# Performance work log

Hardware: AMD Instinct MI355X
Metric: run time of the kernel (lower is better)

Reference implementation:

```python
import jax, jax.numpy as jnp
import numpy as np

T, N, L = 512, 128, 256           # encoder steps, batch, decode steps
KV, VS = 128, 128                 # key_size, value_size
EMB, HID, VOC = 256, 512, 34


def _lstm_cell(x, h, c, W_ih, W_hh, b_ih, b_hh):
    # PyTorch LSTMCell gate order: i, f, g, o
    g = x @ W_ih.T + b_ih + h @ W_hh.T + b_hh
    i, f, gg, o = jnp.split(g, 4, axis=-1)
    c2 = jax.nn.sigmoid(f) * c + jax.nn.sigmoid(i) * jnp.tanh(gg)
    h2 = jax.nn.sigmoid(o) * jnp.tanh(c2)
    return h2, c2


def setup_inputs() -> dict:
    k = jax.random.key(0)
    ks = jax.random.split(k, 16)
    s = 0.05
    return {
        "key": jax.random.normal(ks[0], (T, N, KV), jnp.float32),
        "values": jax.random.normal(ks[1], (T, N, VS), jnp.float32),
        "lens": jax.random.randint(ks[2], (N,), 1, T + 1),
        "text": jax.random.randint(ks[3], (N, L), 0, VOC),
        "emb": jax.random.normal(ks[4], (VOC, EMB), jnp.float32) * s,
        "W_ih1": jax.random.normal(ks[5], (4 * HID, EMB + VS), jnp.float32) * s,
        "W_hh1": jax.random.normal(ks[6], (4 * HID, HID), jnp.float32) * s,
        "b_ih1": jnp.zeros((4 * HID,), jnp.float32),
        "b_hh1": jnp.zeros((4 * HID,), jnp.float32),
        "W_ih2": jax.random.normal(ks[7], (4 * KV, HID), jnp.float32) * s,
        "W_hh2": jax.random.normal(ks[8], (4 * KV, KV), jnp.float32) * s,
        "b_ih2": jnp.zeros((4 * KV,), jnp.float32),
        "b_hh2": jnp.zeros((4 * KV,), jnp.float32),
        "W_out": jax.random.normal(ks[9], (VOC, KV + VS), jnp.float32) * s,
        "b_out": jnp.zeros((VOC,), jnp.float32),
    }


def reference(key, values, lens, text, emb, W_ih1, W_hh1, b_ih1, b_hh1,
              W_ih2, W_hh2, b_ih2, b_hh2, W_out, b_out):
    # key/values: (T, N, 128); teacher-forced decode over L steps.
    pad_mask = jnp.arange(T)[None, :] >= lens[:, None]        # (N, T)
    embs = emb[text]                                          # (N, L, EMB)
    embs = jnp.transpose(embs, (1, 0, 2))                     # (L, N, EMB)

    def step(carry, e_t):
        h1, c1, h2, c2, ctx = carry
        x = jnp.concatenate([e_t, ctx], axis=-1)
        h1, c1 = _lstm_cell(x, h1, c1, W_ih1, W_hh1, b_ih1, b_hh1)
        h2, c2 = _lstm_cell(h1, h2, c2, W_ih2, W_hh2, b_ih2, b_hh2)
        # masked bmm attention: energy (N, T)
        energy = jnp.einsum('tnk,nk->nt', key, h2)
        energy = jnp.where(pad_mask, -1e9, energy)
        attn = jax.nn.softmax(energy, axis=1)
        ctx = jnp.einsum('nt,tnv->nv', attn, values)
        pred = jnp.concatenate([h2, ctx], axis=-1) @ W_out.T + b_out
        return (h1, c1, h2, c2, ctx), pred

    init = (jnp.zeros((N, HID)), jnp.zeros((N, HID)),
            jnp.zeros((N, KV)), jnp.zeros((N, KV)),
            jnp.zeros((N, VS)))
    _, preds = jax.lax.scan(step, init, embs)                 # (L, N, VOC)
    return jnp.transpose(preds, (1, 0, 2))                    # (N, L, VOC)
```

## Files before the change

kernel.cpp:

```cpp
#include <hip/hip_runtime.h>
#include <hip/hip_cooperative_groups.h>
#include <math.h>

#define LDEC 256
#define VOCD 34
#define SPIN_MAX 2000000u

typedef __attribute__((ext_vector_type(8))) short bf16x8;
typedef __attribute__((ext_vector_type(4))) float f32x4;

#define OFF_W1H  0u
#define OFF_W1L  2621440u
#define OFF_W2H  5242880u
#define OFF_W2L  5898240u
#define OFF_EG   6553600u
#define OFF_B2   6832128u
#define OFF_WOT  6834176u
#define OFF_H1P  6868992u
#define OFF_H2P  7393280u
#define OFF_CTXP 7524352u
#define OFF_C1   7589888u
#define OFF_C2   7852032u
#define OFF_FLG  7917568u

__device__ __forceinline__ float sigf(float x) { return 1.0f / (1.0f + expf(-x)); }
__device__ __forceinline__ unsigned short f2b(float x) {
  unsigned int u = __float_as_uint(x);
  unsigned int r = (u + 0x7FFFu + ((u >> 16) & 1u)) >> 16;
  return (unsigned short)r;
}
__device__ __forceinline__ float b2f(unsigned short h) {
  return __uint_as_float(((unsigned int)h) << 16);
}
__device__ __forceinline__ unsigned packf(float x) {
  unsigned short hi = f2b(x);
  unsigned short lo = f2b(x - b2f(hi));
  return ((unsigned)hi << 16) | (unsigned)lo;
}
__device__ __forceinline__ float unpackf(unsigned p) {
  return b2f((unsigned short)(p >> 16)) + b2f((unsigned short)(p & 0xffffu));
}
__device__ __forceinline__ unsigned aload(const unsigned* p) {
  return __hip_atomic_load((unsigned*)p, __ATOMIC_RELAXED, __HIP_MEMORY_SCOPE_SYSTEM);
}
__device__ __forceinline__ void astore(unsigned* p, unsigned v) {
  __hip_atomic_store(p, v, __ATOMIC_RELAXED, __HIP_MEMORY_SCOPE_SYSTEM);
}
__device__ __forceinline__ void unpack8(const unsigned* p, bf16x8& xh, bf16x8& xl) {
#pragma unroll
  for (int j = 0; j < 8; j++) {
    unsigned v = p[j];
    xh[j] = (short)(v >> 16);
    xl[j] = (short)(v & 0xffffu);
  }
}

__device__ __forceinline__ void flag_arrive(unsigned* f) {
  __builtin_amdgcn_s_waitcnt(0);
  __hip_atomic_fetch_add(f, 1u, __ATOMIC_RELAXED, __HIP_MEMORY_SCOPE_SYSTEM);
}
__device__ __forceinline__ void flag_wait(unsigned* f, unsigned target, unsigned* budget) {
  if (*budget == 0) return;
  while (aload(f) < target) {
    __builtin_amdgcn_s_sleep(2);
    if (--(*budget) == 0) break;
  }
  asm volatile("" ::: "memory");
}

__global__ __launch_bounds__(256) void pack_w1(const float* __restrict__ Wih1,
                                               const float* __restrict__ Whh1,
                                               unsigned short* __restrict__ W1H,
                                               unsigned short* __restrict__ W1L) {
  int idx = blockIdx.x * 256 + threadIdx.x;
  int m = idx / 640, k = idx % 640;
  int u = m >> 2, q = m & 3;
  int g = q * 512 + u;
  float v = (k < 128) ? Wih1[g * 384 + 256 + k] : Whh1[g * 512 + (k - 128)];
  unsigned short hi = f2b(v);
  W1H[idx] = hi;
  W1L[idx] = f2b(v - b2f(hi));
}

__global__ __launch_bounds__(256) void pack_w2(const float* __restrict__ Wih2,
                                               const float* __restrict__ Whh2,
                                               unsigned short* __restrict__ W2H,
                                               unsigned short* __restrict__ W2L) {
  int idx = blockIdx.x * 256 + threadIdx.x;
  int m = idx / 640, k = idx % 640;
  int u = m >> 2, q = m & 3;
  int g = q * 128 + u;
  float v = (k < 512) ? Wih2[g * 512 + k] : Whh2[g * 128 + (k - 512)];
  unsigned short hi = f2b(v);
  W2H[idx] = hi;
  W2L[idx] = f2b(v - b2f(hi));
}

__global__ __launch_bounds__(256) void pack_eg(const float* __restrict__ emb,
                                               const float* __restrict__ Wih1,
                                               const float* __restrict__ bih1,
                                               const float* __restrict__ bhh1,
                                               float* __restrict__ EG) {
  int idx = blockIdx.x * 256 + threadIdx.x;
  int v = idx >> 11, m = idx & 2047;
  int u = m >> 2, q = m & 3;
  int g = q * 512 + u;
  float acc = bih1[g] + bhh1[g];
  const float* e = emb + v * 256;
  const float* w = Wih1 + g * 384;
  for (int k = 0; k < 256; k++) acc += e[k] * w[k];
  EG[idx] = acc;
}

__global__ __launch_bounds__(256) void pack_misc(const float* __restrict__ Wout,
                                                 const float* __restrict__ bih2,
                                                 const float* __restrict__ bhh2,
                                                 float* __restrict__ WoT,
                                                 float* __restrict__ B2) {
  int idx = blockIdx.x * 256 + threadIdx.x;
  if (idx < 8704) {
    int k = idx / 34, v = idx % 34;
    WoT[idx] = Wout[v * 256 + k];
  } else if (idx < 9216) {
    int m = idx - 8704;
    int u = m >> 2, q = m & 3;
    int g = q * 128 + u;
    B2[m] = bih2[g] + bhh2[g];
  }
}

__device__ __forceinline__ void dev_phaseA(
    int gang, int gidx, int tid, int t, int rp, int wp,
    const unsigned short* __restrict__ W1H, const unsigned short* __restrict__ W1L,
    const float* __restrict__ EG, const int* __restrict__ text,
    const unsigned* __restrict__ CTXP, unsigned* __restrict__ H1P,
    float* __restrict__ C1)
{
  __shared__ unsigned xsh[16 * 644];
  __shared__ float bredA[4096];

  const int wid = tid >> 6, lane = tid & 63;
  const int l15 = lane & 15, lg = lane >> 4;
  const int gr = wid >> 2, gwid = wid & 3;
  const int kb0 = gwid * 160;

  {
    int kcol = tid & 15, nl = (tid >> 4) & 15, rep = tid >> 8;
    int n = gang * 16 + nl;
    const unsigned* ctxp = CTXP + n * 128;
    const unsigned* h1p  = H1P + rp * 65536 + n * 512;
#pragma unroll
    for (int j = 0; j < 10; j++) {
      int k = rep * 160 + j * 16 + kcol;
      unsigned v = (k < 128) ? aload(ctxp + k) : aload(h1p + (k - 128));
      xsh[nl * 644 + k] = v;
    }
  }
  __syncthreads();

  const int mt = gidx * 4 + gr;
  {
    const unsigned short* whp = W1H + (size_t)(mt * 16 + l15) * 640 + kb0 + lg * 8;
    const unsigned short* wlp = W1L + (size_t)(mt * 16 + l15) * 640 + kb0 + lg * 8;
    const unsigned* xrow = xsh + l15 * 644 + kb0 + lg * 8;
    f32x4 a0 = {0.0f, 0.0f, 0.0f, 0.0f};
    f32x4 a1 = {0.0f, 0.0f, 0.0f, 0.0f};
    f32x4 a2 = {0.0f, 0.0f, 0.0f, 0.0f};
#pragma unroll
    for (int ks = 0; ks < 5; ks++) {
      unsigned parr[8];
      *(uint4*)parr       = *(const uint4*)(xrow + ks * 32);
      *(uint4*)(parr + 4) = *(const uint4*)(xrow + ks * 32 + 4);
      bf16x8 xh_, xl_;
      unpack8(parr, xh_, xl_);
      bf16x8 wh_ = *(const bf16x8*)(whp + ks * 32);
      bf16x8 wl_ = *(const bf16x8*)(wlp + ks * 32);
      a0 = __builtin_amdgcn_mfma_f32_16x16x32_bf16(wh_, xh_, a0, 0, 0, 0);
      a1 = __builtin_amdgcn_mfma_f32_16x16x32_bf16(wl_, xh_, a1, 0, 0, 0);
      a2 = __builtin_amdgcn_mfma_f32_16x16x32_bf16(wh_, xl_, a2, 0, 0, 0);
    }
    f32x4 acc = a0 + a1;
    acc = acc + a2;
#pragma unroll
    for (int q = 0; q < 4; q++) bredA[gr * 1024 + q * 256 + gwid * 64 + lane] = acc[q];
  }
  __syncthreads();

  if (gwid == 0) {
    const float* br = bredA + gr * 1024;
    int n = gang * 16 + l15;
    int tok = text[n * LDEC + t];
    f32x4 egv = *(const f32x4*)(EG + (size_t)tok * 2048 + mt * 16 + lg * 4);
    float g0 = br[lane]       + br[64 + lane]  + br[128 + lane] + br[192 + lane] + egv[0];
    float g1 = br[256 + lane] + br[320 + lane] + br[384 + lane] + br[448 + lane] + egv[1];
    float g2 = br[512 + lane] + br[576 + lane] + br[640 + lane] + br[704 + lane] + egv[2];
    float g3 = br[768 + lane] + br[832 + lane] + br[896 + lane] + br[960 + lane] + egv[3];
    float ig = sigf(g0), fg = sigf(g1), gg = tanhf(g2), og = sigf(g3);
    int u = mt * 4 + lg;
    float c = fg * C1[u * 128 + n] + ig * gg;
    float h = og * tanhf(c);
    C1[u * 128 + n] = c;
    astore(H1P + wp * 65536 + n * 512 + u, packf(h));
  }
  __syncthreads();
}

__device__ __forceinline__ void dev_phaseB(
    int gang, int gidx, int tid, int rp, int wp,
    const unsigned short* __restrict__ W2H, const unsigned short* __restrict__ W2L,
    const float* __restrict__ B2,
    const unsigned* __restrict__ H1P, unsigned* __restrict__ H2P,
    float* __restrict__ C2)
{
  __shared__ float bredB[1024];
  const int wid = tid >> 6, lane = tid & 63;
  const int l15 = lane & 15, lg = lane >> 4;
  const int mtB = gidx;
  if (tid < 256) {
    const int kb0 = wid * 160;
    int n = gang * 16 + l15;
    const unsigned* x1 = H1P + wp * 65536 + n * 512;
    const unsigned* x2 = H2P + rp * 16384 + n * 128;
    const unsigned short* whp = W2H + (size_t)(mtB * 16 + l15) * 640 + kb0 + lg * 8;
    const unsigned short* wlp = W2L + (size_t)(mtB * 16 + l15) * 640 + kb0 + lg * 8;
    f32x4 a0 = {0.0f, 0.0f, 0.0f, 0.0f};
    f32x4 a1 = {0.0f, 0.0f, 0.0f, 0.0f};
    f32x4 a2 = {0.0f, 0.0f, 0.0f, 0.0f};
#pragma unroll
    for (int ks = 0; ks < 5; ks++) {
      int kb = kb0 + ks * 32;
      unsigned parr[8];
      const unsigned* src = (kb < 512) ? (x1 + kb + lg * 8) : (x2 + (kb - 512) + lg * 8);
#pragma unroll
      for (int j = 0; j < 8; j++) parr[j] = aload(src + j);
      bf16x8 xh_, xl_;
      unpack8(parr, xh_, xl_);
      bf16x8 wh_ = *(const bf16x8*)(whp + ks * 32);
      bf16x8 wl_ = *(const bf16x8*)(wlp + ks * 32);
      a0 = __builtin_amdgcn_mfma_f32_16x16x32_bf16(wh_, xh_, a0, 0, 0, 0);
      a1 = __builtin_amdgcn_mfma_f32_16x16x32_bf16(wl_, xh_, a1, 0, 0, 0);
      a2 = __builtin_amdgcn_mfma_f32_16x16x32_bf16(wh_, xl_, a2, 0, 0, 0);
    }
    f32x4 acc = a0 + a1;
    acc = acc + a2;
#pragma unroll
    for (int q = 0; q < 4; q++) bredB[q * 256 + wid * 64 + lane] = acc[q];
  }
  __syncthreads();
  if (tid < 64) {
    f32x4 b2v = *(const f32x4*)(B2 + mtB * 16 + lg * 4);
    float g0 = bredB[lane]       + bredB[64 + lane]  + bredB[128 + lane] + bredB[192 + lane] + b2v[0];
    float g1 = bredB[256 + lane] + bredB[320 + lane] + bredB[384 + lane] + bredB[448 + lane] + b2v[1];
    float g2 = bredB[512 + lane] + bredB[576 + lane] + bredB[640 + lane] + bredB[704 + lane] + b2v[2];
    float g3 = bredB[768 + lane] + bredB[832 + lane] + bredB[896 + lane] + bredB[960 + lane] + b2v[3];
    int n = gang * 16 + l15;
    int u = mtB * 4 + lg;
    float c = sigf(g1) * C2[u * 128 + n] + sigf(g0) * tanhf(g2);
    float h = sigf(g3) * tanhf(c);
    C2[u * 128 + n] = c;
    astore(H2P + wp * 16384 + n * 128 + u, packf(h));
  }
  __syncthreads();
}

__device__ __forceinline__ void dev_phaseC(
    int n, int tid, int len, int t, int wp,
    const float* __restrict__ key, const float* __restrict__ values,
    const unsigned* __restrict__ H2P, const float* __restrict__ WoT,
    const float* __restrict__ bout, unsigned* __restrict__ CTXP,
    float* __restrict__ out)
{
  __shared__ float cred[4224];
  __shared__ float red[1024];
  __shared__ float es[512];
  __shared__ float h2s[128];
  __shared__ float ctxs[128];
  __shared__ float pr[68];

  if (tid < 128) h2s[tid] = unpackf(aload(H2P + wp * 16384 + n * 128 + tid));
  __syncthreads();
  float lmax = -1e30f;
  if (tid < len) {
    const float4* kr = (const float4*)(key + ((size_t)tid * 128 + n) * 128);
    float acc = 0.0f;
#pragma unroll 8
    for (int k = 0; k < 32; k++) {
      float4 kv = kr[k];
      acc += kv.x * h2s[4 * k] + kv.y * h2s[4 * k + 1] + kv.z * h2s[4 * k + 2] + kv.w * h2s[4 * k + 3];
    }
    es[tid] = acc;
    lmax = acc;
  }
  red[tid] = lmax; __syncthreads();
  for (int s = 512; s > 0; s >>= 1) { if (tid < s) red[tid] = fmaxf(red[tid], red[tid + s]); __syncthreads(); }
  float m = red[0];
  __syncthreads();
  float ls = 0.0f;
  if (tid < len) {
    float p = expf(es[tid] - m);
    es[tid] = p;
    ls = p;
  }
  red[tid] = ls; __syncthreads();
  for (int s = 512; s > 0; s >>= 1) { if (tid < s) red[tid] += red[tid + s]; __syncthreads(); }
  float S = red[0];
  __syncthreads();
  {
    int v4 = (tid & 31) * 4, tp = tid >> 5;
    float ax = 0.0f, ay = 0.0f, az = 0.0f, aw = 0.0f;
#pragma unroll 2
    for (int tt = tp; tt < len; tt += 32) {
      float p = es[tt];
      const float4 vv = *(const float4*)(values + ((size_t)tt * 128 + n) * 128 + v4);
      ax += p * vv.x; ay += p * vv.y; az += p * vv.z; aw += p * vv.w;
    }
    float4 a4 = {ax, ay, az, aw};
    *(float4*)&cred[tp * 132 + v4] = a4;
  }
  __syncthreads();
  if (tid < 128) {
    float s4 = 0.0f;
#pragma unroll 8
    for (int tp2 = 0; tp2 < 32; tp2++) s4 += cred[tp2 * 132 + tid];
    float cv = s4 / S;
    ctxs[tid] = cv;
    astore(CTXP + n * 128 + tid, packf(cv));
  }
  __syncthreads();
  if (tid < 68) {
    int vv = tid % 34, part = tid / 34;
    const float* src = part ? ctxs : h2s;
    const float* wcol = WoT + (part ? 128 * 34 : 0);
    float a = 0.0f;
#pragma unroll 8
    for (int k2 = 0; k2 < 128; k2++) a += src[k2] * wcol[k2 * 34 + vv];
    pr[tid] = a;
  }
  __syncthreads();
  if (tid < 34) {
    out[(size_t)n * (LDEC * VOCD) + t * VOCD + tid] = bout[tid] + pr[tid] + pr[34 + tid];
  }
  __syncthreads();
}

__global__ void __launch_bounds__(1024, 4) kA(
    const unsigned short* __restrict__ W1H, const unsigned short* __restrict__ W1L,
    const float* __restrict__ EG, const int* __restrict__ text,
    const unsigned* __restrict__ CTXP, unsigned* __restrict__ H1P,
    float* __restrict__ C1, int t, int rp, int wp)
{
  dev_phaseA(blockIdx.x >> 5, blockIdx.x & 31, threadIdx.x, t, rp, wp,
             W1H, W1L, EG, text, CTXP, H1P, C1);
}
__global__ void __launch_bounds__(256) kB(
    const unsigned short* __restrict__ W2H, const unsigned short* __restrict__ W2L,
    const float* __restrict__ B2, const unsigned* __restrict__ H1P,
    unsigned* __restrict__ H2P, float* __restrict__ C2, int rp, int wp)
{
  dev_phaseB(blockIdx.x >> 5, blockIdx.x & 31, threadIdx.x, rp, wp,
             W2H, W2L, B2, H1P, H2P, C2);
}
__global__ void __launch_bounds__(1024, 4) kC(
    const float* __restrict__ key, const float* __restrict__ values,
    const int* __restrict__ lens, const unsigned* __restrict__ H2P,
    const float* __restrict__ WoT, const float* __restrict__ bout,
    unsigned* __restrict__ CTXP, float* __restrict__ out, int t, int wp)
{
  int n = blockIdx.x;
  dev_phaseC(n, threadIdx.x, lens[n], t, wp, key, values, H2P, WoT, bout, CTXP, out);
}

__global__ void __launch_bounds__(1024, 4) decoder_coop(
    const float* __restrict__ key, const float* __restrict__ values,
    const int* __restrict__ lens, const int* __restrict__ text,
    const float* __restrict__ EG, const float* __restrict__ B2,
    const float* __restrict__ WoT, const float* __restrict__ bout,
    const unsigned short* __restrict__ W1H, const unsigned short* __restrict__ W1L,
    const unsigned short* __restrict__ W2H, const unsigned short* __restrict__ W2L,
    unsigned* __restrict__ CTXP, unsigned* __restrict__ H1P,
    unsigned* __restrict__ H2P, float* __restrict__ C1, float* __restrict__ C2,
    unsigned* __restrict__ FLG, float* __restrict__ out)
{
  const int bid = blockIdx.x, tid = threadIdx.x;
  const int gang = bid >> 5, gidx = bid & 31;
  unsigned* fA = FLG + gang * 16;
  unsigned* fB = FLG + 128 + gang * 16;
  unsigned* fC = FLG + 256 + gang * 16;
  const int cn = gang * 16 + gidx;
  const int clen = (gidx < 16) ? lens[cn] : 0;

  unsigned budget = SPIN_MAX;

  for (int t = 0; t < LDEC; t++) {
    const int wp = t & 1, rp = (t + 1) & 1;

    dev_phaseA(gang, gidx, tid, t, rp, wp, W1H, W1L, EG, text, CTXP, H1P, C1);
    if (tid == 0) { flag_arrive(fA); flag_wait(fA, 32u * (t + 1), &budget); }
    __syncthreads();

    dev_phaseB(gang, gidx, tid, rp, wp, W2H, W2L, B2, H1P, H2P, C2);
    if (tid == 0) flag_arrive(fB);
    if (gidx < 16) {
      if (tid == 0) flag_wait(fB, 32u * (t + 1), &budget);
      __syncthreads();
      dev_phaseC(cn, tid, clen, t, wp, key, values, H2P, WoT, bout, CTXP, out);
      if (tid == 0) flag_arrive(fC);
    }
    if (tid == 0) flag_wait(fC, 16u * (t + 1), &budget);
    __syncthreads();
  }

  if (tid == 0 && budget == 0) out[0] = 7.0e6f;
}

extern "C" void kernel_launch(void* const* d_in, const int* in_sizes, int n_in,
                              void* d_out, int out_size, void* d_ws, size_t ws_size,
                              hipStream_t stream) {
  const float* key    = (const float*)d_in[0];
  const float* values = (const float*)d_in[1];
  const int*   lens   = (const int*)d_in[2];
  const int*   text   = (const int*)d_in[3];
  const float* emb    = (const float*)d_in[4];
  const float* Wih1   = (const float*)d_in[5];
  const float* Whh1   = (const float*)d_in[6];
  const float* bih1   = (const float*)d_in[7];
  const float* bhh1   = (const float*)d_in[8];
  const float* Wih2   = (const float*)d_in[9];
  const float* Whh2   = (const float*)d_in[10];
  const float* bih2   = (const float*)d_in[11];
  const float* bhh2   = (const float*)d_in[12];
  const float* Wout   = (const float*)d_in[13];
  const float* bout   = (const float*)d_in[14];

  char* ws = (char*)d_ws;
  unsigned short* W1H = (unsigned short*)(ws + OFF_W1H);
  unsigned short* W1L = (unsigned short*)(ws + OFF_W1L);
  unsigned short* W2H = (unsigned short*)(ws + OFF_W2H);
  unsigned short* W2L = (unsigned short*)(ws + OFF_W2L);
  float* EG   = (float*)(ws + OFF_EG);
  float* B2   = (float*)(ws + OFF_B2);
  float* WoT  = (float*)(ws + OFF_WOT);
  unsigned* H1P  = (unsigned*)(ws + OFF_H1P);
  unsigned* H2P  = (unsigned*)(ws + OFF_H2P);
  unsigned* CTXP = (unsigned*)(ws + OFF_CTXP);
  float* C1   = (float*)(ws + OFF_C1);
  float* C2   = (float*)(ws + OFF_C2);
  unsigned* FLG = (unsigned*)(ws + OFF_FLG);
  float* out  = (float*)d_out;

  hipMemsetAsync(CTXP, 0, 65536, stream);
  hipMemsetAsync((char*)H1P + 262144, 0, 262144, stream);
  hipMemsetAsync((char*)H2P + 65536, 0, 65536, stream);
  hipMemsetAsync(C1,  0, 262144, stream);
  hipMemsetAsync(C2,  0, 65536, stream);
  hipMemsetAsync(FLG, 0, 2048, stream);

  pack_w1  <<<5120, 256, 0, stream>>>(Wih1, Whh1, W1H, W1L);
  pack_w2  <<<1280, 256, 0, stream>>>(Wih2, Whh2, W2H, W2L);
  pack_eg  <<<272,  256, 0, stream>>>(emb, Wih1, bih1, bhh1, EG);
  pack_misc<<<36,   256, 0, stream>>>(Wout, bih2, bhh2, WoT, B2);

  int maxBlk = 0;
  hipError_t qerr = hipOccupancyMaxActiveBlocksPerMultiprocessor(
      &maxBlk, (const void*)decoder_coop, 1024, 0);
  bool coop_ok = (qerr == hipSuccess && maxBlk >= 1);

  if (coop_ok) {
    void* args[] = {
      (void*)&key, (void*)&values, (void*)&lens, (void*)&text,
      (void*)&EG, (void*)&B2, (void*)&WoT, (void*)&bout,
      (void*)&W1H, (void*)&W1L, (void*)&W2H, (void*)&W2L,
      (void*)&CTXP, (void*)&H1P, (void*)&H2P, (void*)&C1, (void*)&C2,
      (void*)&FLG, (void*)&out
    };
    hipError_t err = hipLaunchCooperativeKernel((const void*)decoder_coop,
                                                dim3(256), dim3(1024), args, 0, stream);
    if (err == hipSuccess) return;
  }

  for (int t = 0; t < LDEC; t++) {
    const int wp = t & 1, rp = (t + 1) & 1;
    kA<<<256, 1024, 0, stream>>>(W1H, W1L, EG, text, CTXP, H1P, C1, t, rp, wp);
    kB<<<256, 256,  0, stream>>>(W2H, W2L, B2, H1P, H2P, C2, rp, wp);
    kC<<<128, 1024, 0, stream>>>(key, values, lens, H2P, WoT, bout, CTXP, out, t, wp);
  }
}
```

Before: 9.203 ms.

## Redistribute LSTM phase work across fewer blocks and prestage h1 into shared memory

Phase A now runs on 16 blocks per gang, each handling two m-tiles, and phase B on 8 blocks per gang using all 16 waves with an LDS-staged input. The next step's h1 is staged into shared memory right after phase A, so it overlaps with the phase-B and phase-C waits, and only the ctx part is reloaded at the start of each step. Phase-C shared buffers are unioned with the phase-B staging buffer to keep LDS within budget. The cost is fewer active blocks per phase, so each participating block does more serial work.

```diff
diff --git a/kernel.cpp b/kernel.cpp
--- a/kernel.cpp
+++ b/kernel.cpp
@@ -129,40 +129,42 @@
   }
 }
 
-__device__ __forceinline__ void dev_phaseA(
-    int gang, int gidx, int tid, int t, int rp, int wp,
+__device__ __forceinline__ void stage_h1(int gang, int tid, int rbuf,
+                                         unsigned* xshA, const unsigned* __restrict__ H1P) {
+  int kcol = tid & 15, nl = (tid >> 4) & 15, rep = tid >> 8;
+  int n = gang * 16 + nl;
+  const unsigned* h1p = H1P + rbuf * 65536 + n * 512;
+#pragma unroll
+  for (int j = 0; j < 10; j++) {
+    int k = rep * 160 + j * 16 + kcol;
+    if (k >= 128) xshA[nl * 644 + k] = aload(h1p + (k - 128));
+  }
+}
+__device__ __forceinline__ void stage_ctx(int gang, int tid,
+                                          unsigned* xshA, const unsigned* __restrict__ CTXP) {
+  int kcol = tid & 15, nl = (tid >> 4) & 15, rep = tid >> 8;
+  int n = gang * 16 + nl;
+  if (rep == 0) {
+#pragma unroll
+    for (int j = 0; j < 8; j++) {
+      int k = j * 16 + kcol;
+      xshA[nl * 644 + k] = aload(CTXP + n * 128 + k);
+    }
+  }
+}
+
+__device__ __forceinline__ void A_tile(
+    int gang, int mt, int gr, int gwid, int lane, int l15, int lg, int tid, int t,
+    const unsigned* __restrict__ xshA, float* bred,
     const unsigned short* __restrict__ W1H, const unsigned short* __restrict__ W1L,
     const float* __restrict__ EG, const int* __restrict__ text,
-    const unsigned* __restrict__ CTXP, unsigned* __restrict__ H1P,
-    float* __restrict__ C1)
-{
-  __shared__ unsigned xsh[16 * 644];
-  __shared__ float bredA[4096];
-
-  const int wid = tid >> 6, lane = tid & 63;
-  const int l15 = lane & 15, lg = lane >> 4;
-  const int gr = wid >> 2, gwid = wid & 3;
+    unsigned* __restrict__ H1P, float* __restrict__ C1, int wp)
+{
   const int kb0 = gwid * 160;
-
-  {
-    int kcol = tid & 15, nl = (tid >> 4) & 15, rep = tid >> 8;
-    int n = gang * 16 + nl;
-    const unsigned* ctxp = CTXP + n * 128;
-    const unsigned* h1p  = H1P + rp * 65536 + n * 512;
-#pragma unroll
-    for (int j = 0; j < 10; j++) {
-      int k = rep * 160 + j * 16 + kcol;
-      unsigned v = (k < 128) ? aload(ctxp + k) : aload(h1p + (k - 128));
-      xsh[nl * 644 + k] = v;
-    }
-  }
-  __syncthreads();
-
-  const int mt = gidx * 4 + gr;
   {
     const unsigned short* whp = W1H + (size_t)(mt * 16 + l15) * 640 + kb0 + lg * 8;
     const unsigned short* wlp = W1L + (size_t)(mt * 16 + l15) * 640 + kb0 + lg * 8;
-    const unsigned* xrow = xsh + l15 * 644 + kb0 + lg * 8;
+    const unsigned* xrow = xshA + l15 * 644 + kb0 + lg * 8;
     f32x4 a0 = {0.0f, 0.0f, 0.0f, 0.0f};
     f32x4 a1 = {0.0f, 0.0f, 0.0f, 0.0f};
     f32x4 a2 = {0.0f, 0.0f, 0.0f, 0.0f};
@@ -182,12 +184,11 @@
     f32x4 acc = a0 + a1;
     acc = acc + a2;
 #pragma unroll
-    for (int q = 0; q < 4; q++) bredA[gr * 1024 + q * 256 + gwid * 64 + lane] = acc[q];
-  }
-  __syncthreads();
-
+    for (int q = 0; q < 4; q++) bred[gr * 1024 + q * 256 + gwid * 64 + lane] = acc[q];
+  }
+  __syncthreads();
   if (gwid == 0) {
-    const float* br = bredA + gr * 1024;
+    const float* br = bred + gr * 1024;
     int n = gang * 16 + l15;
     int tok = text[n * LDEC + t];
     f32x4 egv = *(const f32x4*)(EG + (size_t)tok * 2048 + mt * 16 + lg * 4);
@@ -205,34 +206,26 @@
   __syncthreads();
 }
 
-__device__ __forceinline__ void dev_phaseB(
-    int gang, int gidx, int tid, int rp, int wp,
+__device__ __forceinline__ void B_tile(
+    int gang, int mtB, int gr, int gwid, int lane, int l15, int lg,
+    const unsigned* __restrict__ xshB, float* bred,
     const unsigned short* __restrict__ W2H, const unsigned short* __restrict__ W2L,
-    const float* __restrict__ B2,
-    const unsigned* __restrict__ H1P, unsigned* __restrict__ H2P,
-    float* __restrict__ C2)
-{
-  __shared__ float bredB[1024];
-  const int wid = tid >> 6, lane = tid & 63;
-  const int l15 = lane & 15, lg = lane >> 4;
-  const int mtB = gidx;
-  if (tid < 256) {
-    const int kb0 = wid * 160;
-    int n = gang * 16 + l15;
-    const unsigned* x1 = H1P + wp * 65536 + n * 512;
-    const unsigned* x2 = H2P + rp * 16384 + n * 128;
+    const float* __restrict__ B2, unsigned* __restrict__ H2P,
+    float* __restrict__ C2, int wp)
+{
+  const int kb0 = gwid * 160;
+  {
     const unsigned short* whp = W2H + (size_t)(mtB * 16 + l15) * 640 + kb0 + lg * 8;
     const unsigned short* wlp = W2L + (size_t)(mtB * 16 + l15) * 640 + kb0 + lg * 8;
+    const unsigned* xrow = xshB + l15 * 644 + kb0 + lg * 8;
     f32x4 a0 = {0.0f, 0.0f, 0.0f, 0.0f};
     f32x4 a1 = {0.0f, 0.0f, 0.0f, 0.0f};
     f32x4 a2 = {0.0f, 0.0f, 0.0f, 0.0f};
 #pragma unroll
     for (int ks = 0; ks < 5; ks++) {
-      int kb = kb0 + ks * 32;
       unsigned parr[8];
-      const unsigned* src = (kb < 512) ? (x1 + kb + lg * 8) : (x2 + (kb - 512) + lg * 8);
-#pragma unroll
-      for (int j = 0; j < 8; j++) parr[j] = aload(src + j);
+      *(uint4*)parr       = *(const uint4*)(xrow + ks * 32);
+      *(uint4*)(parr + 4) = *(const uint4*)(xrow + ks * 32 + 4);
       bf16x8 xh_, xl_;
       unpack8(parr, xh_, xl_);
       bf16x8 wh_ = *(const bf16x8*)(whp + ks * 32);
@@ -244,16 +237,17 @@
     f32x4 acc = a0 + a1;
     acc = acc + a2;
 #pragma unroll
-    for (int q = 0; q < 4; q++) bredB[q * 256 + wid * 64 + lane] = acc[q];
-  }
-  __syncthreads();
-  if (tid < 64) {
+    for (int q = 0; q < 4; q++) bred[gr * 1024 + q * 256 + gwid * 64 + lane] = acc[q];
+  }
+  __syncthreads();
+  if (gwid == 0) {
+    const float* br = bred + gr * 1024;
+    int n = gang * 16 + l15;
     f32x4 b2v = *(const f32x4*)(B2 + mtB * 16 + lg * 4);
-    float g0 = bredB[lane]       + bredB[64 + lane]  + bredB[128 + lane] + bredB[192 + lane] + b2v[0];
-    float g1 = bredB[256 + lane] + bredB[320 + lane] + bredB[384 + lane] + bredB[448 + lane] + b2v[1];
-    float g2 = bredB[512 + lane] + bredB[576 + lane] + bredB[640 + lane] + bredB[704 + lane] + b2v[2];
-    float g3 = bredB[768 + lane] + bredB[832 + lane] + bredB[896 + lane] + bredB[960 + lane] + b2v[3];
-    int n = gang * 16 + l15;
+    float g0 = br[lane]       + br[64 + lane]  + br[128 + lane] + br[192 + lane] + b2v[0];
+    float g1 = br[256 + lane] + br[320 + lane] + br[384 + lane] + br[448 + lane] + b2v[1];
+    float g2 = br[512 + lane] + br[576 + lane] + br[640 + lane] + br[704 + lane] + b2v[2];
+    float g3 = br[768 + lane] + br[832 + lane] + br[896 + lane] + br[960 + lane] + b2v[3];
     int u = mtB * 4 + lg;
     float c = sigf(g1) * C2[u * 128 + n] + sigf(g0) * tanhf(g2);
     float h = sigf(g3) * tanhf(c);
@@ -263,20 +257,29 @@
   __syncthreads();
 }
 
+__device__ __forceinline__ void stage_B(int gang, int tid, int rp, int wp,
+                                        unsigned* xshB,
+                                        const unsigned* __restrict__ H1P,
+                                        const unsigned* __restrict__ H2P) {
+  int kcol = tid & 15, nl = (tid >> 4) & 15, rep = tid >> 8;
+  int n = gang * 16 + nl;
+  const unsigned* x1 = H1P + wp * 65536 + n * 512;
+  const unsigned* x2 = H2P + rp * 16384 + n * 128;
+#pragma unroll
+  for (int j = 0; j < 10; j++) {
+    int k = rep * 160 + j * 16 + kcol;
+    xshB[nl * 644 + k] = (k < 512) ? aload(x1 + k) : aload(x2 + (k - 512));
+  }
+}
+
 __device__ __forceinline__ void dev_phaseC(
     int n, int tid, int len, int t, int wp,
+    float* cred, float* red, float* es, float* h2s, float* ctxs, float* pr,
     const float* __restrict__ key, const float* __restrict__ values,
     const unsigned* __restrict__ H2P, const float* __restrict__ WoT,
     const float* __restrict__ bout, unsigned* __restrict__ CTXP,
     float* __restrict__ out)
 {
-  __shared__ float cred[4224];
-  __shared__ float red[1024];
-  __shared__ float es[512];
-  __shared__ float h2s[128];
-  __shared__ float ctxs[128];
-  __shared__ float pr[68];
-
   if (tid < 128) h2s[tid] = unpackf(aload(H2P + wp * 16384 + n * 128 + tid));
   __syncthreads();
   float lmax = -1e30f;
@@ -343,34 +346,64 @@
   __syncthreads();
 }
 
-__global__ void __launch_bounds__(1024, 4) kA(
+struct alignas(16) CUnion {
+  union {
+    unsigned xshB[16 * 644];
+    struct { float cred[4224]; float red[1024]; float es[512]; float h2s[128]; float ctxs[128]; float pr[68]; } c;
+  };
+};
+
+__global__ void __launch_bounds__(1024, 1) kA(
     const unsigned short* __restrict__ W1H, const unsigned short* __restrict__ W1L,
     const float* __restrict__ EG, const int* __restrict__ text,
     const unsigned* __restrict__ CTXP, unsigned* __restrict__ H1P,
     float* __restrict__ C1, int t, int rp, int wp)
 {
-  dev_phaseA(blockIdx.x >> 5, blockIdx.x & 31, threadIdx.x, t, rp, wp,
-             W1H, W1L, EG, text, CTXP, H1P, C1);
-}
-__global__ void __launch_bounds__(256) kB(
+  __shared__ unsigned xshA[16 * 644];
+  __shared__ float bred[4096];
+  const int gang = blockIdx.x >> 4, gidx = blockIdx.x & 15;
+  const int tid = threadIdx.x, wid = tid >> 6, lane = tid & 63;
+  const int l15 = lane & 15, lg = lane >> 4;
+  const int gr = wid >> 2, gwid = wid & 3;
+  stage_h1(gang, tid, rp, xshA, H1P);
+  stage_ctx(gang, tid, xshA, CTXP);
+  __syncthreads();
+  for (int r = 0; r < 2; r++) {
+    int mt = gidx * 8 + r * 4 + gr;
+    A_tile(gang, mt, gr, gwid, lane, l15, lg, tid, t, xshA, bred,
+           W1H, W1L, EG, text, H1P, C1, wp);
+  }
+}
+__global__ void __launch_bounds__(1024, 1) kB(
     const unsigned short* __restrict__ W2H, const unsigned short* __restrict__ W2L,
     const float* __restrict__ B2, const unsigned* __restrict__ H1P,
     unsigned* __restrict__ H2P, float* __restrict__ C2, int rp, int wp)
 {
-  dev_phaseB(blockIdx.x >> 5, blockIdx.x & 31, threadIdx.x, rp, wp,
-             W2H, W2L, B2, H1P, H2P, C2);
-}
-__global__ void __launch_bounds__(1024, 4) kC(
+  __shared__ unsigned xshB[16 * 644];
+  __shared__ float bred[4096];
+  const int gang = blockIdx.x >> 3, gidx = blockIdx.x & 7;
+  const int tid = threadIdx.x, wid = tid >> 6, lane = tid & 63;
+  const int l15 = lane & 15, lg = lane >> 4;
+  const int gr = wid >> 2, gwid = wid & 3;
+  stage_B(gang, tid, rp, wp, xshB, H1P, H2P);
+  __syncthreads();
+  B_tile(gang, gidx * 4 + gr, gr, gwid, lane, l15, lg, xshB, bred,
+         W2H, W2L, B2, H2P, C2, wp);
+}
+__global__ void __launch_bounds__(1024, 1) kC(
     const float* __restrict__ key, const float* __restrict__ values,
     const int* __restrict__ lens, const unsigned* __restrict__ H2P,
     const float* __restrict__ WoT, const float* __restrict__ bout,
     unsigned* __restrict__ CTXP, float* __restrict__ out, int t, int wp)
 {
+  __shared__ CUnion cu;
   int n = blockIdx.x;
-  dev_phaseC(n, threadIdx.x, lens[n], t, wp, key, values, H2P, WoT, bout, CTXP, out);
-}
-
-__global__ void __launch_bounds__(1024, 4) decoder_coop(
+  dev_phaseC(n, threadIdx.x, lens[n], t, wp,
+             cu.c.cred, cu.c.red, cu.c.es, cu.c.h2s, cu.c.ctxs, cu.c.pr,
+             key, values, H2P, WoT, bout, CTXP, out);
+}
+
+__global__ void __launch_bounds__(1024, 1) decoder_coop(
     const float* __restrict__ key, const float* __restrict__ values,
     const int* __restrict__ lens, const int* __restrict__ text,
     const float* __restrict__ EG, const float* __restrict__ B2,
@@ -381,8 +414,15 @@
     unsigned* __restrict__ H2P, float* __restrict__ C1, float* __restrict__ C2,
     unsigned* __restrict__ FLG, float* __restrict__ out)
 {
+  __shared__ unsigned xshA[16 * 644];
+  __shared__ float bred[4096];
+  __shared__ CUnion cu;
+
   const int bid = blockIdx.x, tid = threadIdx.x;
   const int gang = bid >> 5, gidx = bid & 31;
+  const int wid = tid >> 6, lane = tid & 63;
+  const int l15 = lane & 15, lg = lane >> 4;
+  const int gr = wid >> 2, gwid = wid & 3;
   unsigned* fA = FLG + gang * 16;
   unsigned* fB = FLG + 128 + gang * 16;
   unsigned* fC = FLG + 256 + gang * 16;
@@ -391,19 +431,40 @@
 
   unsigned budget = SPIN_MAX;
 
+  if (gidx < 16) stage_h1(gang, tid, 1, xshA, H1P);
+
   for (int t = 0; t < LDEC; t++) {
     const int wp = t & 1, rp = (t + 1) & 1;
 
-    dev_phaseA(gang, gidx, tid, t, rp, wp, W1H, W1L, EG, text, CTXP, H1P, C1);
+    if (gidx < 16) {
+      stage_ctx(gang, tid, xshA, CTXP);
+      __syncthreads();
+#pragma unroll 1
+      for (int r = 0; r < 2; r++) {
+        int mt = gidx * 8 + r * 4 + gr;
+        A_tile(gang, mt, gr, gwid, lane, l15, lg, tid, t, xshA, bred,
+               W1H, W1L, EG, text, H1P, C1, wp);
+      }
+    }
     if (tid == 0) { flag_arrive(fA); flag_wait(fA, 32u * (t + 1), &budget); }
     __syncthreads();
 
-    dev_phaseB(gang, gidx, tid, rp, wp, W2H, W2L, B2, H1P, H2P, C2);
+    if (gidx < 16) stage_h1(gang, tid, wp, xshA, H1P);
+
+    if (gidx < 8) {
+      stage_B(gang, tid, rp, wp, cu.xshB, H1P, H2P);
+      __syncthreads();
+      B_tile(gang, gidx * 4 + gr, gr, gwid, lane, l15, lg, cu.xshB, bred,
+             W2H, W2L, B2, H2P, C2, wp);
+    }
     if (tid == 0) flag_arrive(fB);
+
     if (gidx < 16) {
       if (tid == 0) flag_wait(fB, 32u * (t + 1), &budget);
       __syncthreads();
-      dev_phaseC(cn, tid, clen, t, wp, key, values, H2P, WoT, bout, CTXP, out);
+      dev_phaseC(cn, tid, clen, t, wp,
+                 cu.c.cred, cu.c.red, cu.c.es, cu.c.h2s, cu.c.ctxs, cu.c.pr,
+                 key, values, H2P, WoT, bout, CTXP, out);
       if (tid == 0) flag_arrive(fC);
     }
     if (tid == 0) flag_wait(fC, 16u * (t + 1), &budget);
@@ -480,8 +541,8 @@
 
   for (int t = 0; t < LDEC; t++) {
     const int wp = t & 1, rp = (t + 1) & 1;
-    kA<<<256, 1024, 0, stream>>>(W1H, W1L, EG, text, CTXP, H1P, C1, t, rp, wp);
-    kB<<<256, 256,  0, stream>>>(W2H, W2L, B2, H1P, H2P, C2, rp, wp);
+    kA<<<128, 1024, 0, stream>>>(W1H, W1L, EG, text, CTXP, H1P, C1, t, rp, wp);
+    kB<<<64,  1024, 0, stream>>>(W2H, W2L, B2, H1P, H2P, C2, rp, wp);
     kC<<<128, 1024, 0, stream>>>(key, values, lens, H2P, WoT, bout, CTXP, out, t, wp);
   }
 }
```

Result: slower. 11.15 ms (+21.1%).
